# Performance work log

Measured on AMD Instinct MI355X. Metric: run time of the kernel, lower is better.

## Reference

```python
import jax, jax.numpy as jnp
import numpy as np

D = 256; NH = 8; HD = D // NH; L = 4; P = 4; NQ = 900; BS = 8; DFFN = 1024
SHAPES = np.array([[128, 128], [64, 64], [32, 32], [16, 16]])  # (H, W) per level, static metadata
NV = int((SHAPES[:, 0] * SHAPES[:, 1]).sum())
EPS = 1e-6


def setup_inputs():
    key = jax.random.key(0)
    ks = iter(jax.random.split(key, 48))

    def nrm(shape, scale=0.02):
        return jax.random.normal(next(ks), shape, jnp.float32) * scale

    lsi = np.concatenate([[0], np.cumsum(SHAPES[:, 0] * SHAPES[:, 1])[:-1]]).astype(np.int64)
    return {
        'tgt': nrm((NQ, BS, D), 1.0),
        'tgt_query_pos': nrm((NQ, BS, D), 1.0),
        'tgt_reference_points': jax.random.uniform(next(ks), (NQ, BS, L, 2), jnp.float32),
        'memory': nrm((NV, BS, D), 1.0),
        'memory_spatial_shapes': jnp.asarray(SHAPES, jnp.int32),
        'memory_level_start_index': jnp.asarray(lsi, jnp.int32),
        'w_norm_sa': jnp.ones((D,), jnp.float32),
        'w_norm_ca': jnp.ones((D,), jnp.float32),
        'w_norm_ffn': jnp.ones((D,), jnp.float32),
        'ls_sa': jnp.full((D,), 1e-4, jnp.float32),
        'ls_ca': jnp.full((D,), 1e-4, jnp.float32),
        'ls_ffn': jnp.full((D,), 1e-4, jnp.float32),
        'Wq': nrm((D, D)), 'Wk': nrm((D, D)), 'Wv': nrm((D, D)),
        'bq': jnp.zeros((D,), jnp.float32), 'bk': jnp.zeros((D,), jnp.float32), 'bv': jnp.zeros((D,), jnp.float32),
        'Wo_sa': nrm((D, D)), 'bo_sa': jnp.zeros((D,), jnp.float32),
        'Wv_proj': nrm((D, D)), 'bv_proj': jnp.zeros((D,), jnp.float32),
        'W_off': nrm((NH * L * P * 2, D)), 'b_off': nrm((NH * L * P * 2,), 0.1),
        'W_attn': nrm((NH * L * P, D)), 'b_attn': jnp.zeros((NH * L * P,), jnp.float32),
        'W_out_ca': nrm((D, D)), 'bo_ca': jnp.zeros((D,), jnp.float32),
        'Wg': nrm((DFFN, D)), 'bg': jnp.zeros((DFFN,), jnp.float32),
        'Wu': nrm((DFFN, D)), 'bu': jnp.zeros((DFFN,), jnp.float32),
        'Wf': nrm((D, DFFN)), 'bf': jnp.zeros((D,), jnp.float32),
    }


def rmsnorm(x, w):
    return x * jax.lax.rsqrt(jnp.mean(x * x, axis=-1, keepdims=True) + EPS) * w


def ms_deform_sample(v, loc, attw):
    # v: (bs, nv, NH, HD); loc: (bs, nq, NH, L, P, 2) normalized (x, y); attw: (bs, nq, NH, L, P)
    bs, nq = loc.shape[0], loc.shape[1]
    out = jnp.zeros((bs, nq, NH, HD), loc.dtype)
    b_idx = jnp.arange(bs)[:, None, None, None]
    h_idx = jnp.arange(NH)[None, None, :, None]
    start = 0
    for l in range(L):
        Hl, Wl = int(SHAPES[l, 0]), int(SHAPES[l, 1])
        vf = v[:, start:start + Hl * Wl]  # (bs, Hl*Wl, NH, HD)
        start += Hl * Wl
        # grid_sample(align_corners=False, padding=zeros) pixel mapping
        x = loc[:, :, :, l, :, 0] * Wl - 0.5
        y = loc[:, :, :, l, :, 1] * Hl - 0.5
        x0 = jnp.floor(x)
        y0 = jnp.floor(y)
        acc = jnp.zeros((bs, nq, NH, P, HD), loc.dtype)
        for dx in (0, 1):
            for dy in (0, 1):
                xi = x0 + dx
                yi = y0 + dy
                w = (1.0 - jnp.abs(x - xi)) * (1.0 - jnp.abs(y - yi))
                valid = (xi >= 0) & (xi <= Wl - 1) & (yi >= 0) & (yi <= Hl - 1)
                w = jnp.where(valid, w, 0.0)
                idx = (jnp.clip(yi, 0, Hl - 1) * Wl + jnp.clip(xi, 0, Wl - 1)).astype(jnp.int32)
                acc = acc + w[..., None] * vf[b_idx, idx, h_idx]  # (bs, nq, NH, P, HD)
        out = out + jnp.einsum('bqhp,bqhpd->bqhd', attw[:, :, :, l], acc)
    return out


def reference(tgt, tgt_query_pos, tgt_reference_points, memory, memory_spatial_shapes,
              memory_level_start_index, w_norm_sa, w_norm_ca, w_norm_ffn, ls_sa, ls_ca, ls_ffn,
              Wq, Wk, Wv, bq, bk, bv, Wo_sa, bo_sa, Wv_proj, bv_proj, W_off, b_off, W_attn,
              b_attn, W_out_ca, bo_ca, Wg, bg, Wu, bu, Wf, bf):
    nq, bs, d = tgt.shape
    # --- self-attention (pre-norm + LayerScale residual) ---
    xn = rmsnorm(tgt, w_norm_sa)
    qk = xn + tgt_query_pos
    q = (qk @ Wq.T + bq).reshape(nq, bs, NH, HD)
    k = (qk @ Wk.T + bk).reshape(nq, bs, NH, HD)
    vv = (xn @ Wv.T + bv).reshape(nq, bs, NH, HD)
    scores = jnp.einsum('qbhd,kbhd->bhqk', q, k) * (1.0 / np.sqrt(HD))
    attn = jax.nn.softmax(scores, axis=-1)
    sa = jnp.einsum('bhqk,kbhd->qbhd', attn, vv).reshape(nq, bs, d) @ Wo_sa.T + bo_sa
    tgt = tgt + ls_sa * sa
    # --- multi-scale deformable cross-attention (identity=zeros in original) ---
    xn = rmsnorm(tgt, w_norm_ca)
    qca = jnp.swapaxes(xn + tgt_query_pos, 0, 1)  # (bs, nq, d)
    val = (jnp.swapaxes(memory, 0, 1) @ Wv_proj.T + bv_proj).reshape(bs, -1, NH, HD)
    off = (qca @ W_off.T + b_off).reshape(bs, nq, NH, L, P, 2)
    attw = jax.nn.softmax((qca @ W_attn.T + b_attn).reshape(bs, nq, NH, L * P), axis=-1)
    attw = attw.reshape(bs, nq, NH, L, P)
    norm = jnp.asarray(SHAPES[:, ::-1].copy(), jnp.float32)  # (W, H) per level
    ref = jnp.swapaxes(tgt_reference_points, 0, 1)  # (bs, nq, L, 2)
    loc = ref[:, :, None, :, None, :] + off / norm[None, None, None, :, None, :]
    ca = ms_deform_sample(val, loc, attw).reshape(bs, nq, d) @ W_out_ca.T + bo_ca
    tgt = tgt + ls_ca * jnp.swapaxes(ca, 0, 1)
    # --- SwiGLU FFN ---
    xn = rmsnorm(tgt, w_norm_ffn)
    ffn = (jax.nn.silu(xn @ Wg.T + bg) * (xn @ Wu.T + bu)) @ Wf.T + bf
    return tgt + ls_ffn * ffn
```

## Files before the change

### kernel.cpp

```cpp
#include <hip/hip_runtime.h>

typedef unsigned short ushort_t;
typedef unsigned int uint32;
typedef __bf16 bf16x8 __attribute__((ext_vector_type(8)));
typedef float f32x4 __attribute__((ext_vector_type(4)));
typedef ushort_t us4 __attribute__((ext_vector_type(4)));

#define D_    256
#define NH_   8
#define HD_   32
#define NQ_   900
#define BS_   8
#define TOK_  7200
#define NV_   21760
#define QP_   928
#define DFFN_ 1024

__device__ __forceinline__ ushort_t f2bf(float x) {
    union { float f; uint32 u; } v; v.f = x;
    uint32 r = v.u + 0x7FFFu + ((v.u >> 16) & 1u);
    return (ushort_t)(r >> 16);
}
__device__ __forceinline__ float bf2f(ushort_t h) {
    union { uint32 u; float f; } v; v.u = ((uint32)h) << 16;
    return v.f;
}
__device__ __forceinline__ int imin(int a, int b) { return a < b ? a : b; }
__device__ __forceinline__ int imax(int a, int b) { return a > b ? a : b; }

__global__ __launch_bounds__(256) void cvtall_k(
    const float* __restrict__ s0, const float* __restrict__ s1, const float* __restrict__ s2,
    const float* __restrict__ s3, const float* __restrict__ s4, const float* __restrict__ s5,
    const float* __restrict__ s6, const float* __restrict__ s7, const float* __restrict__ s8,
    const float* __restrict__ s9, const float* __restrict__ s10, ushort_t* __restrict__ dst,
    const float* __restrict__ bq, const float* __restrict__ bk,
    const float* __restrict__ boff, const float* __restrict__ battn,
    float* __restrict__ bias_qk, float* __restrict__ bias_ol) {
    int tid = threadIdx.x;
    if (blockIdx.x == 0) {
        bias_qk[tid] = bq[tid];
        bias_qk[256 + tid] = bk[tid];
        bias_ol[tid] = boff[tid];
        if (tid < 128) bias_ol[256 + tid] = battn[tid];
    }
    int id = blockIdx.x * 256 + tid;
    const float* s; int off;
    if      (id <  16384) { s = s0;  off = id; }
    else if (id <  32768) { s = s1;  off = id - 16384; }
    else if (id <  49152) { s = s2;  off = id - 32768; }
    else if (id <  65536) { s = s3;  off = id - 49152; }
    else if (id <  81920) { s = s4;  off = id - 65536; }
    else if (id <  98304) { s = s5;  off = id - 81920; }
    else if (id < 114688) { s = s6;  off = id - 98304; }
    else if (id < 122880) { s = s7;  off = id - 114688; }
    else if (id < 188416) { s = s8;  off = id - 122880; }
    else if (id < 253952) { s = s9;  off = id - 188416; }
    else                  { s = s10; off = id - 253952; }
    f32x4 v = *(const f32x4*)(s + (size_t)off * 4);
    us4 t;
#pragma unroll
    for (int e = 0; e < 4; e++) t[e] = f2bf(v[e]);
    *(us4*)(dst + (size_t)id * 4) = t;
}

__global__ __launch_bounds__(256) void rms_k(const float* __restrict__ x,
                                             const float* __restrict__ pos,
                                             const float* __restrict__ wn,
                                             ushort_t* __restrict__ xn_out,
                                             ushort_t* __restrict__ qk_out) {
    int r = blockIdx.x, tid = threadIdx.x;
    float v = x[r * D_ + tid];
    float ss = v * v;
#pragma unroll
    for (int o = 32; o; o >>= 1) ss += __shfl_xor(ss, o, 64);
    __shared__ float part[4];
    if ((tid & 63) == 0) part[tid >> 6] = ss;
    __syncthreads();
    float tot = part[0] + part[1] + part[2] + part[3];
    float sc = rsqrtf(tot * (1.f / 256.f) + 1e-6f);
    float xn = v * sc * wn[tid];
    if (xn_out) xn_out[r * D_ + tid] = f2bf(xn);
    if (qk_out) qk_out[r * D_ + tid] = f2bf(xn + pos[r * D_ + tid]);
}

enum { EPI_RESID, EPI_QK2, EPI_VT, EPI_VAL, EPI_OFFLOG };

template <int EPI, bool AF32, int BM, int BN, int WGM, int WGN, int TK>
__global__ __launch_bounds__(WGM * WGN * 64) void gemm2_k(
    const void* __restrict__ Ap, const ushort_t* __restrict__ Wp,
    const float* __restrict__ bias, void* __restrict__ outp, void* __restrict__ outp2,
    int M, int N, int swz,
    const float* __restrict__ resid, const float* __restrict__ ls, float scale) {
    constexpr int THREADS = WGM * WGN * 64;
    constexpr int NK  = TK / 32;
    constexpr int LDK = 40;
    constexpr int WR  = BM / WGM, WC = BN / WGN;
    constexpr int FM  = WR / 16,  FN = WC / 16;
    constexpr int ACH = AF32 ? (BM * 32 / 4 / THREADS) : (BM * 32 / 8 / THREADS);
    constexpr int BCH = BN * 32 / 8 / THREADS;

    __shared__ __align__(16) ushort_t As[2][BM * LDK];
    __shared__ __align__(16) ushort_t Bs[2][BN * LDK];

    const int tid = threadIdx.x, l = tid & 63, w = tid >> 6;
    const int wm = w % WGM, wn = w / WGM;
    int by = blockIdx.y;
    if (swz) { int cpx = gridDim.y >> 3; by = (by & 7) * cpx + (by >> 3); }
    const int m0 = by * BM, n0 = blockIdx.x * BN;
    const int lr = l & 15, lkb = (l >> 4) * 8;

    const ushort_t* Ab = (const ushort_t*)Ap;
    const float*    Af = (const float*)Ap;

    int aRow[ACH], aK[ACH], bRow[BCH], bK[BCH];
#pragma unroll
    for (int ch = 0; ch < ACH; ch++) {
        int cid = ch * THREADS + tid;
        if constexpr (AF32) { aRow[ch] = cid >> 3; aK[ch] = (cid & 7) * 4; }
        else                { aRow[ch] = cid >> 2; aK[ch] = (cid & 3) * 8; }
    }
#pragma unroll
    for (int ch = 0; ch < BCH; ch++) {
        int cid = ch * THREADS + tid;
        bRow[ch] = cid >> 2; bK[ch] = (cid & 3) * 8;
    }
    int aGRow[ACH];
#pragma unroll
    for (int ch = 0; ch < ACH; ch++) aGRow[ch] = imin(m0 + aRow[ch], M - 1);

    f32x4  aSTf[AF32 ? ACH : 1];
    bf16x8 aSTb[AF32 ? 1 : ACH];
    bf16x8 bST[BCH];

    auto load_regs = [&](int kt) {
        const int k0 = kt * 32;
#pragma unroll
        for (int ch = 0; ch < ACH; ch++) {
            if constexpr (AF32)
                aSTf[ch] = *(const f32x4*)(Af + (size_t)aGRow[ch] * TK + k0 + aK[ch]);
            else
                aSTb[ch] = *(const bf16x8*)(Ab + (size_t)aGRow[ch] * TK + k0 + aK[ch]);
        }
#pragma unroll
        for (int ch = 0; ch < BCH; ch++)
            bST[ch] = *(const bf16x8*)(Wp + (size_t)(n0 + bRow[ch]) * TK + k0 + bK[ch]);
    };
    auto write_lds = [&](int buf) {
#pragma unroll
        for (int ch = 0; ch < ACH; ch++) {
            if constexpr (AF32) {
                us4 t;
#pragma unroll
                for (int e = 0; e < 4; e++) t[e] = f2bf(aSTf[ch][e]);
                *(us4*)&As[buf][aRow[ch] * LDK + aK[ch]] = t;
            } else {
                *(bf16x8*)&As[buf][aRow[ch] * LDK + aK[ch]] = aSTb[ch];
            }
        }
#pragma unroll
        for (int ch = 0; ch < BCH; ch++)
            *(bf16x8*)&Bs[buf][bRow[ch] * LDK + bK[ch]] = bST[ch];
    };

    f32x4 acc[FM][FN];
#pragma unroll
    for (int i = 0; i < FM; i++)
#pragma unroll
        for (int j = 0; j < FN; j++) acc[i][j] = f32x4{0.f, 0.f, 0.f, 0.f};

    load_regs(0);
    write_lds(0);
    __syncthreads();

    for (int kt = 0; kt < NK; ++kt) {
        const int c = kt & 1;
        if (kt + 1 < NK) load_regs(kt + 1);

        bf16x8 af[FM], bf_[FN];
#pragma unroll
        for (int i = 0; i < FM; i++)
            af[i] = *(const bf16x8*)&As[c][(wm * WR + i * 16 + lr) * LDK + lkb];
#pragma unroll
        for (int j = 0; j < FN; j++)
            bf_[j] = *(const bf16x8*)&Bs[c][(wn * WC + j * 16 + lr) * LDK + lkb];
#pragma unroll
        for (int i = 0; i < FM; i++)
#pragma unroll
            for (int j = 0; j < FN; j++)
                acc[i][j] = __builtin_amdgcn_mfma_f32_16x16x32_bf16(af[i], bf_[j], acc[i][j], 0, 0, 0);

        if (kt + 1 < NK) write_lds(c ^ 1);
        __syncthreads();
    }

#pragma unroll
    for (int i = 0; i < FM; i++)
#pragma unroll
        for (int j = 0; j < FN; j++) {
            int col = n0 + wn * WC + j * 16 + lr;
            float bvv = bias[col];
#pragma unroll
            for (int e = 0; e < 4; e++) {
                int row = m0 + wm * WR + i * 16 + (l >> 4) * 4 + e;
                if (row >= M) continue;
                float v = acc[i][j][e] + bvv;
                if constexpr (EPI == EPI_RESID) {
                    size_t idx = (size_t)row * N + col;
                    ((float*)outp)[idx] = resid[idx] + ls[col] * v;
                } else if constexpr (EPI == EPI_QK2) {
                    int c2 = col & 255;
                    int q = row >> 3, bb = row & 7, h = c2 >> 5, hd = c2 & 31;
                    ushort_t* dst = (col < 256) ? (ushort_t*)outp : (ushort_t*)outp2;
                    float sc = (col < 256) ? scale : 1.f;
                    dst[((bb * NH_ + h) * QP_ + q) * HD_ + hd] = f2bf(v * sc);
                } else if constexpr (EPI == EPI_VT) {
                    int q = row >> 3, bb = row & 7, h = col >> 5, hd = col & 31;
                    ((ushort_t*)outp)[((bb * NH_ + h) * HD_ + hd) * QP_ + q] = f2bf(v);
                } else if constexpr (EPI == EPI_VAL) {
                    int vv = row >> 3, bb = row & 7, h = col >> 5, d = col & 31;
                    ((ushort_t*)outp)[(((size_t)(bb * NH_ + h)) * NV_ + vv) * HD_ + d] = f2bf(v);
                } else if constexpr (EPI == EPI_OFFLOG) {
                    if (col < 256) ((float*)outp)[(size_t)row * 256 + col] = v;
                    else           ((float*)outp2)[(size_t)row * 128 + col - 256] = v;
                }
            }
        }
}

__global__ __launch_bounds__(512, 4) void gemm3_k(
    const float* __restrict__ Af, const ushort_t* __restrict__ Wp,
    const float* __restrict__ bias, ushort_t* __restrict__ outp, int swz) {
    constexpr int TK = 256, NK = 8, LDK = 264;
    __shared__ __align__(16) ushort_t Bs[128 * LDK];

    const int tid = threadIdx.x, l = tid & 63, w = tid >> 6;
    const int wm = w & 3, wn = w >> 2;
    int by = blockIdx.y;
    if (swz) { int cpx = gridDim.y >> 3; by = (by & 7) * cpx + (by >> 3); }
    const int m0 = by * 128, n0 = blockIdx.x * 128;
    const int lr = l & 15, g = l >> 4, lkb = g * 8;

    {
        const int r2 = tid >> 5, c2 = (tid & 31) * 8;
#pragma unroll
        for (int ch = 0; ch < 8; ch++) {
            bf16x8 t = *(const bf16x8*)(Wp + (size_t)(n0 + r2 + ch * 16) * TK + c2);
            *(bf16x8*)&Bs[(r2 + ch * 16) * LDK + c2] = t;
        }
    }
    __syncthreads();

    const int arow = m0 + wm * 32 + lr;
    const float* aBase = Af + (size_t)arow * TK + lkb;

    f32x4 aC[2][2];
#pragma unroll
    for (int i = 0; i < 2; i++) {
        const f32x4* p = (const f32x4*)(aBase + (size_t)i * 16 * TK);
        aC[i][0] = p[0]; aC[i][1] = p[1];
    }

    f32x4 acc[2][4];
#pragma unroll
    for (int i = 0; i < 2; i++)
#pragma unroll
        for (int j = 0; j < 4; j++) acc[i][j] = f32x4{0.f, 0.f, 0.f, 0.f};

    for (int kt = 0; kt < NK; ++kt) {
        f32x4 aN[2][2];
        if (kt + 1 < NK) {
#pragma unroll
            for (int i = 0; i < 2; i++) {
                const f32x4* p = (const f32x4*)(aBase + (size_t)i * 16 * TK + (kt + 1) * 32);
                aN[i][0] = p[0]; aN[i][1] = p[1];
            }
        }
        bf16x8 af[2];
#pragma unroll
        for (int i = 0; i < 2; i++)
#pragma unroll
            for (int e = 0; e < 4; e++) {
                af[i][e]     = (__bf16)aC[i][0][e];
                af[i][4 + e] = (__bf16)aC[i][1][e];
            }
        bf16x8 bfr[4];
#pragma unroll
        for (int j = 0; j < 4; j++)
            bfr[j] = *(const bf16x8*)&Bs[(wn * 64 + j * 16 + lr) * LDK + kt * 32 + lkb];
#pragma unroll
        for (int i = 0; i < 2; i++)
#pragma unroll
            for (int j = 0; j < 4; j++)
                acc[i][j] = __builtin_amdgcn_mfma_f32_16x16x32_bf16(af[i], bfr[j], acc[i][j], 0, 0, 0);
#pragma unroll
        for (int i = 0; i < 2; i++) { aC[i][0] = aN[i][0]; aC[i][1] = aN[i][1]; }
    }

#pragma unroll
    for (int i = 0; i < 2; i++)
#pragma unroll
        for (int j = 0; j < 4; j++) {
            int col = n0 + wn * 64 + j * 16 + lr;
            float bvv = bias[col];
            int h = col >> 5, d = col & 31;
#pragma unroll
            for (int e = 0; e < 4; e++) {
                int row = m0 + wm * 32 + i * 16 + g * 4 + e;
                int vv = row >> 3, bb = row & 7;
                float v = acc[i][j][e] + bvv;
                outp[(((size_t)(bb * NH_ + h)) * NV_ + vv) * HD_ + d] = f2bf(v);
            }
        }
}

__global__ __launch_bounds__(256) void ffn_k(
    const ushort_t* __restrict__ Ap, const ushort_t* __restrict__ Wg,
    const ushort_t* __restrict__ Wu, const float* __restrict__ bgp,
    const float* __restrict__ bup, ushort_t* __restrict__ outp, int M) {
    constexpr int BM = 64, BN = 128, TK = 256, NK = TK / 32, LDK = 40;
    constexpr int WR = 32, WC = 64, FM = 2, FN = 4;

    __shared__ __align__(16) ushort_t As[2][BM * LDK];
    __shared__ __align__(16) ushort_t Gs[2][BN * LDK];
    __shared__ __align__(16) ushort_t Us[2][BN * LDK];

    const int tid = threadIdx.x, l = tid & 63, w = tid >> 6;
    const int wm = w & 1, wn = w >> 1;
    const int m0 = blockIdx.y * BM, n0 = blockIdx.x * BN;
    const int lr = l & 15, lkb = (l >> 4) * 8;

    const int aRow = tid >> 2, aK = (tid & 3) * 8;
    int bRow[2], bK[2];
#pragma unroll
    for (int ch = 0; ch < 2; ch++) { int cid = ch * 256 + tid; bRow[ch] = cid >> 2; bK[ch] = (cid & 3) * 8; }
    const int aGRow = imin(m0 + aRow, M - 1);

    bf16x8 aST, gST[2], uST[2];
    auto load_regs = [&](int kt) {
        const int k0 = kt * 32;
        aST = *(const bf16x8*)(Ap + (size_t)aGRow * TK + k0 + aK);
#pragma unroll
        for (int ch = 0; ch < 2; ch++) {
            gST[ch] = *(const bf16x8*)(Wg + (size_t)(n0 + bRow[ch]) * TK + k0 + bK[ch]);
            uST[ch] = *(const bf16x8*)(Wu + (size_t)(n0 + bRow[ch]) * TK + k0 + bK[ch]);
        }
    };
    auto write_lds = [&](int buf) {
        *(bf16x8*)&As[buf][aRow * LDK + aK] = aST;
#pragma unroll
        for (int ch = 0; ch < 2; ch++) {
            *(bf16x8*)&Gs[buf][bRow[ch] * LDK + bK[ch]] = gST[ch];
            *(bf16x8*)&Us[buf][bRow[ch] * LDK + bK[ch]] = uST[ch];
        }
    };

    f32x4 accG[FM][FN], accU[FM][FN];
#pragma unroll
    for (int i = 0; i < FM; i++)
#pragma unroll
        for (int j = 0; j < FN; j++) { accG[i][j] = f32x4{0,0,0,0}; accU[i][j] = f32x4{0,0,0,0}; }

    load_regs(0);
    write_lds(0);
    __syncthreads();

    for (int kt = 0; kt < NK; ++kt) {
        const int c = kt & 1;
        if (kt + 1 < NK) load_regs(kt + 1);
        bf16x8 af[FM], gf[FN], uf[FN];
#pragma unroll
        for (int i = 0; i < FM; i++)
            af[i] = *(const bf16x8*)&As[c][(wm * WR + i * 16 + lr) * LDK + lkb];
#pragma unroll
        for (int j = 0; j < FN; j++) {
            gf[j] = *(const bf16x8*)&Gs[c][(wn * WC + j * 16 + lr) * LDK + lkb];
            uf[j] = *(const bf16x8*)&Us[c][(wn * WC + j * 16 + lr) * LDK + lkb];
        }
#pragma unroll
        for (int i = 0; i < FM; i++)
#pragma unroll
            for (int j = 0; j < FN; j++) {
                accG[i][j] = __builtin_amdgcn_mfma_f32_16x16x32_bf16(af[i], gf[j], accG[i][j], 0, 0, 0);
                accU[i][j] = __builtin_amdgcn_mfma_f32_16x16x32_bf16(af[i], uf[j], accU[i][j], 0, 0, 0);
            }
        if (kt + 1 < NK) write_lds(c ^ 1);
        __syncthreads();
    }

#pragma unroll
    for (int i = 0; i < FM; i++)
#pragma unroll
        for (int j = 0; j < FN; j++) {
            int col = n0 + wn * WC + j * 16 + lr;
            float bg_ = bgp[col], bu_ = bup[col];
#pragma unroll
            for (int e = 0; e < 4; e++) {
                int row = m0 + wm * WR + i * 16 + (l >> 4) * 4 + e;
                if (row >= M) continue;
                float g = accG[i][j][e] + bg_;
                float u = accU[i][j][e] + bu_;
                float s = g / (1.f + __expf(-g));
                outp[(size_t)row * DFFN_ + col] = f2bf(s * u);
            }
        }
}

__global__ __launch_bounds__(256) void attn2_k(const ushort_t* __restrict__ qb,
                                               const ushort_t* __restrict__ kb,
                                               const ushort_t* __restrict__ vtb,
                                               ushort_t* __restrict__ sab) {
    __shared__ __align__(16) ushort_t Pl[4][16 * 40];
    const int tid = threadIdx.x, l = tid & 63, w = tid >> 6;
    const int bh = blockIdx.y, b = bh >> 3, h = bh & 7;
    const int q0 = (blockIdx.x * 4 + w) * 16;
    if (q0 >= NQ_) return;
    const int q = l & 15, g = l >> 4;
    ushort_t* Pw = &Pl[w][0];

    const bf16x8 qf = *(const bf16x8*)(qb + ((size_t)bh * QP_ + q0 + q) * HD_ + g * 8);
    const ushort_t* kbase = kb + (size_t)bh * QP_ * HD_;
    const ushort_t* vbase = vtb + (size_t)bh * HD_ * QP_;

    f32x4 O0 = {0.f, 0.f, 0.f, 0.f}, O1 = {0.f, 0.f, 0.f, 0.f};
    float m = -1e30f, sl = 0.f;

    auto ldk = [&](int t, int u) {
        return *(const bf16x8*)(kbase + (size_t)(t * 32 + u * 16 + q) * HD_ + g * 8);
    };
    auto ldv = [&](int t, int dh) {
        return *(const bf16x8*)(vbase + (size_t)(dh * 16 + q) * QP_ + t * 32 + g * 8);
    };
    bf16x8 kA = ldk(0, 0), kB = ldk(0, 1), v0 = ldv(0, 0), v1 = ldv(0, 1);

    for (int t = 0; t < 29; ++t) {
        bf16x8 nkA, nkB, nv0, nv1;
        if (t < 28) { nkA = ldk(t + 1, 0); nkB = ldk(t + 1, 1); nv0 = ldv(t + 1, 0); nv1 = ldv(t + 1, 1); }
        const f32x4 z = {0.f, 0.f, 0.f, 0.f};
        f32x4 sA = __builtin_amdgcn_mfma_f32_16x16x32_bf16(kA, qf, z, 0, 0, 0);
        f32x4 sB = __builtin_amdgcn_mfma_f32_16x16x32_bf16(kB, qf, z, 0, 0, 0);
        if (t == 28) {
            int k0 = 896 + g * 4;
#pragma unroll
            for (int e = 0; e < 4; e++) {
                if (k0 + e >= NQ_)      sA[e] = -1e30f;
                if (k0 + 16 + e >= NQ_) sB[e] = -1e30f;
            }
        }
        float tm = fmaxf(fmaxf(fmaxf(sA[0], sA[1]), fmaxf(sA[2], sA[3])),
                         fmaxf(fmaxf(sB[0], sB[1]), fmaxf(sB[2], sB[3])));
        tm = fmaxf(tm, __shfl_xor(tm, 16, 64));
        tm = fmaxf(tm, __shfl_xor(tm, 32, 64));
        float mn = fmaxf(m, tm);
        float r = exp2f(m - mn);
        m = mn;
#pragma unroll
        for (int e = 0; e < 4; e++) { O0[e] *= r; O1[e] *= r; }
        float pA[4], pB[4], ps = 0.f;
#pragma unroll
        for (int e = 0; e < 4; e++) {
            pA[e] = exp2f(sA[e] - m); pB[e] = exp2f(sB[e] - m);
            ps += pA[e] + pB[e];
        }
        sl = sl * r + ps;
        uint32 a0, a1, b0, b1;
        asm("v_cvt_pk_bf16_f32 %0, %1, %2" : "=v"(a0) : "v"(pA[0]), "v"(pA[1]));
        asm("v_cvt_pk_bf16_f32 %0, %1, %2" : "=v"(a1) : "v"(pA[2]), "v"(pA[3]));
        asm("v_cvt_pk_bf16_f32 %0, %1, %2" : "=v"(b0) : "v"(pB[0]), "v"(pB[1]));
        asm("v_cvt_pk_bf16_f32 %0, %1, %2" : "=v"(b1) : "v"(pB[2]), "v"(pB[3]));
        { uint2 tt; tt.x = a0; tt.y = a1; *(uint2*)(Pw + q * 40 + g * 4) = tt; }
        { uint2 tt; tt.x = b0; tt.y = b1; *(uint2*)(Pw + q * 40 + 16 + g * 4) = tt; }
        bf16x8 pf = *(const bf16x8*)(Pw + q * 40 + g * 8);
        O0 = __builtin_amdgcn_mfma_f32_16x16x32_bf16(v0, pf, O0, 0, 0, 0);
        O1 = __builtin_amdgcn_mfma_f32_16x16x32_bf16(v1, pf, O1, 0, 0, 0);
        kA = nkA; kB = nkB; v0 = nv0; v1 = nv1;
    }

    sl += __shfl_xor(sl, 16, 64);
    sl += __shfl_xor(sl, 32, 64);
    float inv = 1.f / sl;
    int row_q = q0 + q;
    if (row_q < NQ_) {
        ushort_t* op = sab + ((size_t)row_q * BS_ + b) * D_ + h * HD_ + g * 4;
#pragma unroll
        for (int dh = 0; dh < 2; dh++) {
            f32x4 Ov = dh ? O1 : O0;
            float e0 = Ov[0] * inv, e1 = Ov[1] * inv, e2 = Ov[2] * inv, e3 = Ov[3] * inv;
            uint32 w0, w1;
            asm("v_cvt_pk_bf16_f32 %0, %1, %2" : "=v"(w0) : "v"(e0), "v"(e1));
            asm("v_cvt_pk_bf16_f32 %0, %1, %2" : "=v"(w1) : "v"(e2), "v"(e3));
            *(uint32*)(op + dh * 16) = w0;
            *(uint32*)(op + dh * 16 + 2) = w1;
        }
    }
}

__global__ __launch_bounds__(256) void deform_k(
    const float* __restrict__ offb, const float* __restrict__ logb,
    const float* __restrict__ refpts, const int* __restrict__ shapes,
    const int* __restrict__ lsi, const ushort_t* __restrict__ val,
    ushort_t* __restrict__ ca) {
    __shared__ float off_l[256];
    __shared__ float attw[128];
    const int r = blockIdx.x;
    const int b = r & 7;
    const int tid = threadIdx.x;

    off_l[tid] = offb[(size_t)r * 256 + tid];
    if (tid < 128) {
        float lg = logb[(size_t)r * 128 + tid];
        float m = lg;
#pragma unroll
        for (int o = 1; o < 16; o <<= 1) m = fmaxf(m, __shfl_xor(m, o, 16));
        float e = __expf(lg - m);
        float s = e;
#pragma unroll
        for (int o = 1; o < 16; o <<= 1) s += __shfl_xor(s, o, 16);
        attw[tid] = e / s;
    }
    __syncthreads();

    const int h = tid >> 5, d = tid & 31;
    const ushort_t* vb = val + ((size_t)(b * NH_ + h)) * NV_ * HD_;
    float acc = 0.f;
#pragma unroll
    for (int lvl = 0; lvl < 4; lvl++) {
        const int H = shapes[lvl * 2], W = shapes[lvl * 2 + 1];
        const int base = lsi[lvl];
        const float refx = refpts[(r * 4 + lvl) * 2];
        const float refy = refpts[(r * 4 + lvl) * 2 + 1];
#pragma unroll
        for (int p = 0; p < 4; p++) {
            int oi = ((h * 4 + lvl) * 4 + p) * 2;
            float x = (refx + off_l[oi] / (float)W) * (float)W - 0.5f;
            float y = (refy + off_l[oi + 1] / (float)H) * (float)H - 0.5f;
            float x0 = floorf(x), y0 = floorf(y);
            float fx = x - x0, fy = y - y0;
            int ix = (int)x0, iy = (int)y0;
            float sval = 0.f;
#pragma unroll
            for (int dy = 0; dy <= 1; dy++)
#pragma unroll
                for (int dx = 0; dx <= 1; dx++) {
                    int xi = ix + dx, yi = iy + dy;
                    float wq = (dx ? fx : 1.f - fx) * (dy ? fy : 1.f - fy);
                    if (xi < 0 || xi >= W || yi < 0 || yi >= H) wq = 0.f;
                    int cx = imin(imax(xi, 0), W - 1), cy = imin(imax(yi, 0), H - 1);
                    float vv = bf2f(vb[(size_t)(base + cy * W + cx) * HD_ + d]);
                    sval += wq * vv;
                }
            acc += attw[h * 16 + lvl * 4 + p] * sval;
        }
    }
    ca[(size_t)r * 256 + tid] = f2bf(acc);
}

extern "C" void kernel_launch(void* const* d_in, const int* in_sizes, int n_in,
                              void* d_out, int out_size, void* d_ws, size_t ws_size,
                              hipStream_t stream) {
    (void)in_sizes; (void)n_in; (void)out_size; (void)ws_size;
    const float* tgt    = (const float*)d_in[0];
    const float* qpos   = (const float*)d_in[1];
    const float* refp   = (const float*)d_in[2];
    const float* mem    = (const float*)d_in[3];
    const int*   shapes = (const int*)d_in[4];
    const int*   lsi    = (const int*)d_in[5];
    const float* wnsa   = (const float*)d_in[6];
    const float* wnca   = (const float*)d_in[7];
    const float* wnffn  = (const float*)d_in[8];
    const float* lssa   = (const float*)d_in[9];
    const float* lsca   = (const float*)d_in[10];
    const float* lsffn  = (const float*)d_in[11];
    const float* Wq = (const float*)d_in[12];
    const float* Wk = (const float*)d_in[13];
    const float* Wv = (const float*)d_in[14];
    const float* bq = (const float*)d_in[15];
    const float* bk = (const float*)d_in[16];
    const float* bvv = (const float*)d_in[17];
    const float* Wo_sa = (const float*)d_in[18];
    const float* bo_sa = (const float*)d_in[19];
    const float* Wv_proj = (const float*)d_in[20];
    const float* bv_proj = (const float*)d_in[21];
    const float* W_off = (const float*)d_in[22];
    const float* b_off = (const float*)d_in[23];
    const float* W_attn = (const float*)d_in[24];
    const float* b_attn = (const float*)d_in[25];
    const float* W_out = (const float*)d_in[26];
    const float* bo_ca = (const float*)d_in[27];
    const float* Wg = (const float*)d_in[28];
    const float* bg = (const float*)d_in[29];
    const float* Wu = (const float*)d_in[30];
    const float* bu = (const float*)d_in[31];
    const float* Wf = (const float*)d_in[32];
    const float* bff = (const float*)d_in[33];

    char* ws = (char*)d_ws;
    size_t o = 0;
    auto alloc = [&](size_t b) { size_t c = o; o += (b + 255) & ~(size_t)255; return c; };

    const size_t wq_o = alloc(65536 * 2), wk_o = alloc(65536 * 2), wv_o = alloc(65536 * 2);
    const size_t wosa_o = alloc(65536 * 2), wvp_o = alloc(65536 * 2), wout_o = alloc(65536 * 2);
    const size_t woff_o = alloc(65536 * 2), wattn_o = alloc(32768 * 2);
    const size_t wg_o = alloc(262144 * 2), wu_o = alloc(262144 * 2), wf_o = alloc(262144 * 2);
    const size_t bqk_o = alloc(512 * 4), bol_o = alloc(384 * 4);
    const size_t xnsa_o = alloc((size_t)TOK_ * D_ * 2);
    const size_t qksa_o = alloc((size_t)TOK_ * D_ * 2);
    const size_t qkvBytes = (size_t)BS_ * NH_ * QP_ * HD_ * 2;
    const size_t qb_o = alloc(qkvBytes);
    const size_t kb_o = alloc(qkvBytes);
    const size_t vt_o = alloc(qkvBytes + 512);
    const size_t sa_o = alloc((size_t)TOK_ * D_ * 2);
    const size_t tgt1_o = alloc((size_t)TOK_ * D_ * 4);
    const size_t qca_o = alloc((size_t)TOK_ * D_ * 2);
    const size_t offb_o = alloc((size_t)TOK_ * 256 * 4);
    const size_t logit_o = alloc((size_t)TOK_ * 128 * 4);
    const size_t ca_o = alloc((size_t)TOK_ * D_ * 2);
    const size_t tgt2_o = alloc((size_t)TOK_ * D_ * 4);
    const size_t val_o = alloc((size_t)NV_ * BS_ * D_ * 2);
    const size_t h_o  = val_o;
    const size_t xn3_o = h_o + (size_t)TOK_ * DFFN_ * 2;

    dim3 blk(256);
    cvtall_k<<<dim3(319488 / 256), blk, 0, stream>>>(
        Wq, Wk, Wv, Wo_sa, Wv_proj, W_out, W_off, W_attn, Wg, Wu, Wf,
        (ushort_t*)(ws + wq_o),
        bq, bk, b_off, b_attn, (float*)(ws + bqk_o), (float*)(ws + bol_o));

    (void)hipMemsetAsync(ws + vt_o, 0, qkvBytes + 512, stream);

    rms_k<<<dim3(TOK_), blk, 0, stream>>>(tgt, qpos, wnsa,
                                          (ushort_t*)(ws + xnsa_o), (ushort_t*)(ws + qksa_o));
    const float QSC = 0.25503321550239915f;
    gemm2_k<EPI_QK2, false, 64, 128, 2, 2, 256><<<dim3(4, 113), blk, 0, stream>>>(
        ws + qksa_o, (ushort_t*)(ws + wq_o), (const float*)(ws + bqk_o),
        ws + qb_o, ws + kb_o, TOK_, 512, 0, nullptr, nullptr, QSC);
    gemm2_k<EPI_VT, false, 64, 128, 2, 2, 256><<<dim3(2, 113), blk, 0, stream>>>(
        ws + xnsa_o, (ushort_t*)(ws + wv_o), bvv, ws + vt_o, nullptr, TOK_, 256, 0,
        nullptr, nullptr, 1.f);
    attn2_k<<<dim3(15, 64), blk, 0, stream>>>((ushort_t*)(ws + qb_o), (ushort_t*)(ws + kb_o),
                                              (ushort_t*)(ws + vt_o), (ushort_t*)(ws + sa_o));
    gemm2_k<EPI_RESID, false, 64, 128, 2, 2, 256><<<dim3(2, 113), blk, 0, stream>>>(
        ws + sa_o, (ushort_t*)(ws + wosa_o), bo_sa, ws + tgt1_o, nullptr, TOK_, 256, 0,
        tgt, lssa, 1.f);

    rms_k<<<dim3(TOK_), blk, 0, stream>>>((const float*)(ws + tgt1_o), qpos, wnca,
                                          nullptr, (ushort_t*)(ws + qca_o));
    gemm2_k<EPI_OFFLOG, false, 64, 128, 2, 2, 256><<<dim3(3, 113), blk, 0, stream>>>(
        ws + qca_o, (ushort_t*)(ws + woff_o), (const float*)(ws + bol_o),
        ws + offb_o, ws + logit_o, TOK_, 384, 0, nullptr, nullptr, 1.f);
    gemm3_k<<<dim3(2, 1360), dim3(512), 0, stream>>>(
        mem, (ushort_t*)(ws + wvp_o), bv_proj, (ushort_t*)(ws + val_o), 1);
    deform_k<<<dim3(TOK_), blk, 0, stream>>>(
        (const float*)(ws + offb_o), (const float*)(ws + logit_o), refp, shapes, lsi,
        (ushort_t*)(ws + val_o), (ushort_t*)(ws + ca_o));
    gemm2_k<EPI_RESID, false, 64, 128, 2, 2, 256><<<dim3(2, 113), blk, 0, stream>>>(
        ws + ca_o, (ushort_t*)(ws + wout_o), bo_ca, ws + tgt2_o, nullptr, TOK_, 256, 0,
        (const float*)(ws + tgt1_o), lsca, 1.f);

    rms_k<<<dim3(TOK_), blk, 0, stream>>>((const float*)(ws + tgt2_o), nullptr, wnffn,
                                          (ushort_t*)(ws + xn3_o), nullptr);
    ffn_k<<<dim3(8, 113), blk, 0, stream>>>(
        (const ushort_t*)(ws + xn3_o), (const ushort_t*)(ws + wg_o),
        (const ushort_t*)(ws + wu_o), bg, bu, (ushort_t*)(ws + h_o), TOK_);
    gemm2_k<EPI_RESID, false, 64, 128, 2, 2, 1024><<<dim3(2, 113), blk, 0, stream>>>(
        ws + h_o, (ushort_t*)(ws + wf_o), bff, d_out, nullptr, TOK_, 256, 0,
        (const float*)(ws + tgt2_o), lsffn, 1.f);
}
```

Baseline: 388.6 us.

## Restructure value-projection GEMM to stage converted A tile in LDS, full N per block

The memory value-projection GEMM now has each block cover all 256 output columns for 128 rows, instead of two blocks per row tile each re-reading the fp32 memory rows. The fp32 A tile is converted to bf16 once and stored in XOR-swizzled shared memory, while weight fragments stream from global/L2 with register double-buffering. This halves the reads and conversions of the large fp32 memory input. The cost is larger LDS per block (64KB), which lowers occupancy, and more accumulators per wave.

Measured after the change: 368.9 us. 1.05x faster.

```diff
diff --git a/kernel.cpp b/kernel.cpp
--- a/kernel.cpp
+++ b/kernel.cpp
@@ -230,82 +230,76 @@
 __global__ __launch_bounds__(512, 4) void gemm3_k(
     const float* __restrict__ Af, const ushort_t* __restrict__ Wp,
     const float* __restrict__ bias, ushort_t* __restrict__ outp, int swz) {
-    constexpr int TK = 256, NK = 8, LDK = 264;
-    __shared__ __align__(16) ushort_t Bs[128 * LDK];
+    constexpr int TK = 256, NK = 8;
+    __shared__ __align__(16) ushort_t As[128 * 256];
 
     const int tid = threadIdx.x, l = tid & 63, w = tid >> 6;
-    const int wm = w & 3, wn = w >> 2;
+    const int wm = w & 1, wn = w >> 1;
     int by = blockIdx.y;
     if (swz) { int cpx = gridDim.y >> 3; by = (by & 7) * cpx + (by >> 3); }
-    const int m0 = by * 128, n0 = blockIdx.x * 128;
-    const int lr = l & 15, g = l >> 4, lkb = g * 8;
-
-    {
-        const int r2 = tid >> 5, c2 = (tid & 31) * 8;
-#pragma unroll
-        for (int ch = 0; ch < 8; ch++) {
-            bf16x8 t = *(const bf16x8*)(Wp + (size_t)(n0 + r2 + ch * 16) * TK + c2);
-            *(bf16x8*)&Bs[(r2 + ch * 16) * LDK + c2] = t;
-        }
+    const int m0 = by * 128;
+    const int lr = l & 15, g = l >> 4;
+
+#pragma unroll
+    for (int ch = 0; ch < 8; ch++) {
+        int c = ch * 512 + tid;
+        int row = c >> 5, cg = c & 31;
+        const f32x4* p = (const f32x4*)(Af + ((size_t)(m0 + row)) * TK + cg * 8);
+        f32x4 p0 = p[0], p1 = p[1];
+        bf16x8 t;
+#pragma unroll
+        for (int e = 0; e < 4; e++) { t[e] = (__bf16)p0[e]; t[4 + e] = (__bf16)p1[e]; }
+        int cgs = cg ^ (row & 7);
+        *(bf16x8*)&As[row * 256 + cgs * 8] = t;
     }
     __syncthreads();
 
-    const int arow = m0 + wm * 32 + lr;
-    const float* aBase = Af + (size_t)arow * TK + lkb;
-
-    f32x4 aC[2][2];
-#pragma unroll
-    for (int i = 0; i < 2; i++) {
-        const f32x4* p = (const f32x4*)(aBase + (size_t)i * 16 * TK);
-        aC[i][0] = p[0]; aC[i][1] = p[1];
-    }
-
-    f32x4 acc[2][4];
-#pragma unroll
-    for (int i = 0; i < 2; i++)
+    const int swzkey = lr & 7;
+    const ushort_t* wBase = Wp + (size_t)(wn * 64 + lr) * TK + g * 8;
+
+    f32x4 acc[4][4];
+#pragma unroll
+    for (int i = 0; i < 4; i++)
 #pragma unroll
         for (int j = 0; j < 4; j++) acc[i][j] = f32x4{0.f, 0.f, 0.f, 0.f};
 
+    bf16x8 bC[4], bN[4];
+#pragma unroll
+    for (int j = 0; j < 4; j++)
+        bC[j] = *(const bf16x8*)(wBase + (size_t)j * 16 * TK);
+
     for (int kt = 0; kt < NK; ++kt) {
-        f32x4 aN[2][2];
         if (kt + 1 < NK) {
 #pragma unroll
-            for (int i = 0; i < 2; i++) {
-                const f32x4* p = (const f32x4*)(aBase + (size_t)i * 16 * TK + (kt + 1) * 32);
-                aN[i][0] = p[0]; aN[i][1] = p[1];
-            }
-        }
-        bf16x8 af[2];
-#pragma unroll
-        for (int i = 0; i < 2; i++)
-#pragma unroll
-            for (int e = 0; e < 4; e++) {
-                af[i][e]     = (__bf16)aC[i][0][e];
-                af[i][4 + e] = (__bf16)aC[i][1][e];
-            }
-        bf16x8 bfr[4];
-#pragma unroll
-        for (int j = 0; j < 4; j++)
-            bfr[j] = *(const bf16x8*)&Bs[(wn * 64 + j * 16 + lr) * LDK + kt * 32 + lkb];
-#pragma unroll
-        for (int i = 0; i < 2; i++)
-#pragma unroll
             for (int j = 0; j < 4; j++)
-                acc[i][j] = __builtin_amdgcn_mfma_f32_16x16x32_bf16(af[i], bfr[j], acc[i][j], 0, 0, 0);
-#pragma unroll
-        for (int i = 0; i < 2; i++) { aC[i][0] = aN[i][0]; aC[i][1] = aN[i][1]; }
-    }
-
-#pragma unroll
-    for (int i = 0; i < 2; i++)
+                bN[j] = *(const bf16x8*)(wBase + (size_t)j * 16 * TK + (kt + 1) * 32);
+        }
+        bf16x8 af[4];
+#pragma unroll
+        for (int i = 0; i < 4; i++) {
+            int row = wm * 64 + i * 16 + lr;
+            int cg = (kt * 4 + g) ^ swzkey;
+            af[i] = *(const bf16x8*)&As[row * 256 + cg * 8];
+        }
+#pragma unroll
+        for (int i = 0; i < 4; i++)
+#pragma unroll
+            for (int j = 0; j < 4; j++)
+                acc[i][j] = __builtin_amdgcn_mfma_f32_16x16x32_bf16(af[i], bC[j], acc[i][j], 0, 0, 0);
+#pragma unroll
+        for (int j = 0; j < 4; j++) bC[j] = bN[j];
+    }
+
+#pragma unroll
+    for (int i = 0; i < 4; i++)
 #pragma unroll
         for (int j = 0; j < 4; j++) {
-            int col = n0 + wn * 64 + j * 16 + lr;
+            int col = wn * 64 + j * 16 + lr;
             float bvv = bias[col];
             int h = col >> 5, d = col & 31;
 #pragma unroll
             for (int e = 0; e < 4; e++) {
-                int row = m0 + wm * 32 + i * 16 + g * 4 + e;
+                int row = m0 + wm * 64 + i * 16 + g * 4 + e;
                 int vv = row >> 3, bb = row & 7;
                 float v = acc[i][j][e] + bvv;
                 outp[(((size_t)(bb * NH_ + h)) * NV_ + vv) * HD_ + d] = f2bf(v);
@@ -647,7 +641,7 @@
     gemm2_k<EPI_OFFLOG, false, 64, 128, 2, 2, 256><<<dim3(3, 113), blk, 0, stream>>>(
         ws + qca_o, (ushort_t*)(ws + woff_o), (const float*)(ws + bol_o),
         ws + offb_o, ws + logit_o, TOK_, 384, 0, nullptr, nullptr, 1.f);
-    gemm3_k<<<dim3(2, 1360), dim3(512), 0, stream>>>(
+    gemm3_k<<<dim3(1, 1360), dim3(512), 0, stream>>>(
         mem, (ushort_t*)(ws + wvp_o), bv_proj, (ushort_t*)(ws + val_o), 1);
     deform_k<<<dim3(TOK_), blk, 0, stream>>>(
         (const float*)(ws + offb_o), (const float*)(ws + logit_o), refp, shapes, lsi,
```
